# Kernel tuning notes

Measured on AMD Instinct MI355X. Metric: run time of the kernel, lower is better.

Reference implementation:

```python
import jax, jax.numpy as jnp
import numpy as np
import math

H = 16
D = 1024
DH = D // H  # 64


def setup_inputs() -> dict:
    key = jax.random.key(0)
    ks = jax.random.split(key, 11)
    B, N = 2, 2048
    f = lambda k, shape, s=1.0: jax.random.normal(k, shape, dtype=jnp.float32) * s
    return {
        "x_q": f(ks[0], (B, N, D)),
        "x_k": f(ks[1], (B, N, D)),
        "x_v": f(ks[2], (B, N, D)),
        "Wq": f(ks[3], (D, D), 0.02),
        "bq": f(ks[4], (D,), 0.02),
        "Wk": f(ks[5], (D, D), 0.02),
        "bk": f(ks[6], (D,), 0.02),
        "Wv": f(ks[7], (D, D), 0.02),
        "bv": f(ks[8], (D,), 0.02),
        "Wo": f(ks[9], (D, D), 0.02),
        "bo": f(ks[10], (D,), 0.02),
    }


def _mha(x_q, x_k, x_v, Wq, bq, Wk, bk, Wv, bv, Wo, bo):
    B, N, _ = x_q.shape
    # torch nn.Linear: y = x @ W.T + b
    def proj(x, W, b):
        y = x @ W.T + b                      # [B, N, D]
        return y.reshape(B, N, H, DH).transpose(0, 2, 1, 3)  # [B, H, N, DH]
    Q = proj(x_q, Wq, bq)
    K = proj(x_k, Wk, bk)
    V = proj(x_v, Wv, bv)
    scores = jnp.einsum("bhqd,bhkd->bhqk", Q, K) / math.sqrt(DH)  # [B,H,N,N]
    attn = jax.nn.softmax(scores, axis=-1)
    X = jnp.einsum("bhqk,bhkd->bhqd", attn, V)   # [B,H,N,DH]
    X = X.transpose(0, 2, 1, 3).reshape(B, N, D)  # concat heads
    return X @ Wo.T + bo


def reference(x_q, x_k, x_v, Wq, bq, Wk, bk, Wv, bv, Wo, bo):
    return _mha(x_q, x_k, x_v, Wq, bq, Wk, bk, Wv, bv, Wo, bo)
```

## Files before the change

kernel.cpp:

```cpp
#include <hip/hip_runtime.h>

typedef unsigned short u16;
typedef __attribute__((ext_vector_type(8))) short s16x8;
typedef __attribute__((ext_vector_type(4))) float f32x4;
typedef unsigned uint2v __attribute__((ext_vector_type(2)));

#define B_  2
#define N_  2048
#define D_  1024
#define H_  16
#define DH_ 64
#define M_  4096

#define S_X (M_ * D_)
#define S_W (D_ * D_)

#define QSCALE 0.1803368801111204f

#define OFF_QB 0
#define OFF_KB (S_X)
#define OFF_VB (2 * S_X)
#define OFF_XB (3 * S_X)
#define OFF_XQ (4 * S_X)
#define OFF_XK (5 * S_X)
#define OFF_XV (6 * S_X)
#define OFF_WQ (7 * S_X)
#define OFF_WK (7 * S_X + S_W)
#define OFF_WV (7 * S_X + 2 * S_W)
#define OFF_WO (7 * S_X + 3 * S_W)
#define WS_FAST_BYTES ((size_t)(7 * S_X + 4 * S_W) * 2)

#if __has_builtin(__builtin_amdgcn_exp2f)
#define EXP2(x) __builtin_amdgcn_exp2f(x)
#else
#define EXP2(x) exp2f(x)
#endif

__device__ __forceinline__ u16 f2bf(float f) {
  unsigned u = __builtin_bit_cast(unsigned, f);
  u += 0x7fffu + ((u >> 16) & 1u);
  return (u16)(u >> 16);
}
__device__ __forceinline__ s16x8 pack8(float4 a, float4 b) {
  s16x8 r;
  r[0] = (short)f2bf(a.x); r[1] = (short)f2bf(a.y);
  r[2] = (short)f2bf(a.z); r[3] = (short)f2bf(a.w);
  r[4] = (short)f2bf(b.x); r[5] = (short)f2bf(b.y);
  r[6] = (short)f2bf(b.z); r[7] = (short)f2bf(b.w);
  return r;
}
__device__ __forceinline__ void gl2lds16(const void* g, void* l) {
  __builtin_amdgcn_global_load_lds(
      (const __attribute__((address_space(1))) void*)g,
      (__attribute__((address_space(3))) void*)l, 16, 0, 0);
}
__device__ __forceinline__ void pl32(unsigned &a, unsigned &b) {
#if __has_builtin(__builtin_amdgcn_permlane32_swap)
  uint2v r = __builtin_amdgcn_permlane32_swap(a, b, 0, 0);
  a = r[0]; b = r[1];
#else
  asm("v_permlane32_swap_b32 %0, %1" : "+v"(a), "+v"(b));
#endif
}
__device__ __forceinline__ void pl16(unsigned &a, unsigned &b) {
#if __has_builtin(__builtin_amdgcn_permlane16_swap)
  uint2v r = __builtin_amdgcn_permlane16_swap(a, b, 0, 0);
  a = r[0]; b = r[1];
#else
  asm("v_permlane16_swap_b32 %0, %1" : "+v"(a), "+v"(b));
#endif
}

__global__ __launch_bounds__(256)
void cvt_kernel(const float* __restrict__ p0, const float* __restrict__ p1,
                const float* __restrict__ p2, const float* __restrict__ p3,
                const float* __restrict__ p4, const float* __restrict__ p5,
                const float* __restrict__ p6, u16* __restrict__ ws) {
  const float* src; u16* dst; int n;
  switch (blockIdx.y) {
    case 0:  src = p0; dst = ws + OFF_XQ; n = S_X; break;
    case 1:  src = p1; dst = ws + OFF_XK; n = S_X; break;
    case 2:  src = p2; dst = ws + OFF_XV; n = S_X; break;
    case 3:  src = p3; dst = ws + OFF_WQ; n = S_W; break;
    case 4:  src = p4; dst = ws + OFF_WK; n = S_W; break;
    case 5:  src = p5; dst = ws + OFF_WV; n = S_W; break;
    default: src = p6; dst = ws + OFF_WO; n = S_W; break;
  }
  const int stride = gridDim.x * blockDim.x * 4;
  for (int idx = (blockIdx.x * blockDim.x + threadIdx.x) * 4; idx < n; idx += stride) {
    const float4 v = *(const float4*)&src[idx];
    ushort4 o;
    o.x = f2bf(v.x); o.y = f2bf(v.y); o.z = f2bf(v.z); o.w = f2bf(v.w);
    *(ushort4*)&dst[idx] = o;
  }
}

__global__ __launch_bounds__(256, 3)
void qkv_gemm_bf(const u16* __restrict__ ws_in, const float* __restrict__ bq,
                 const float* __restrict__ bk, const float* __restrict__ bv,
                 u16* __restrict__ ws_out) {
  __shared__ __align__(16) u16 As[128 * 32];
  __shared__ __align__(16) u16 Bs[128 * 32];
  __shared__ __align__(16) u16 Ts[128][136];
  const int flat = (blockIdx.z * 32 + blockIdx.y) * 8 + blockIdx.x;
  const int u = flat & 7, v = flat >> 3;
  const int bxn = v & 7;
  const int byz = u * 12 + (v >> 3);
  const int z = byz >> 5, bym = byz & 31;

  const u16* A = ws_in + OFF_XQ + (size_t)z * S_X;
  const u16* W = ws_in + OFF_WQ + (size_t)z * S_W;
  const float* bias = (z == 0) ? bq : (z == 1) ? bk : bv;
  u16* out = ws_out + (size_t)z * S_X;
  const float scale = (z == 0) ? QSCALE : 1.0f;

  const int tid  = threadIdx.x;
  const int wave = tid >> 6, lane = tid & 63;
  const int quad = lane >> 4, l16 = lane & 15;
  const int wr = wave >> 1, wc = wave & 1;
  const int m0 = bym * 128, n0 = bxn * 128;

  f32x4 acc[4][4];
#pragma unroll
  for (int i = 0; i < 4; ++i)
#pragma unroll
    for (int j = 0; j < 4; ++j) acc[i][j] = {0.f, 0.f, 0.f, 0.f};

  for (int kt = 0; kt < D_ / 32; ++kt) {
    const int kb = kt * 32;
#pragma unroll
    for (int call = 0; call < 2; ++call) {
      const int c = call * 256 + wave * 64 + lane;
      const int row = c >> 2, col8 = (c & 3) * 8;
      gl2lds16(&A[(size_t)(m0 + row) * D_ + kb + col8],
               &As[(size_t)(call * 256 + wave * 64) * 8]);
      gl2lds16(&W[(size_t)(n0 + row) * D_ + kb + col8],
               &Bs[(size_t)(call * 256 + wave * 64) * 8]);
    }
    __syncthreads();

    s16x8 af[4], bf[4];
#pragma unroll
    for (int i = 0; i < 4; ++i) {
      af[i] = *(const s16x8*)&As[(wr * 64 + i * 16 + l16) * 32 + quad * 8];
      bf[i] = *(const s16x8*)&Bs[(wc * 64 + i * 16 + l16) * 32 + quad * 8];
    }
#pragma unroll
    for (int i = 0; i < 4; ++i)
#pragma unroll
      for (int j = 0; j < 4; ++j)
        acc[i][j] = __builtin_amdgcn_mfma_f32_16x16x32_bf16(af[i], bf[j], acc[i][j], 0, 0, 0);
    __syncthreads();
  }

  if (z != 2) {
#pragma unroll
    for (int j = 0; j < 4; ++j) {
      const int col = n0 + wc * 64 + j * 16 + l16;
      const float bvv = bias[col];
#pragma unroll
      for (int i = 0; i < 4; ++i) {
        const int row0 = m0 + wr * 64 + i * 16 + quad * 4;
#pragma unroll
        for (int r = 0; r < 4; ++r)
          out[(size_t)(row0 + r) * D_ + col] = f2bf((acc[i][j][r] + bvv) * scale);
      }
    }
  } else {
#pragma unroll
    for (int j = 0; j < 4; ++j) {
      const int cl = wc * 64 + j * 16 + l16;
      const float bvv = bias[n0 + cl];
#pragma unroll
      for (int i = 0; i < 4; ++i) {
        const int tl0 = wr * 64 + i * 16 + quad * 4;
#pragma unroll
        for (int r = 0; r < 4; ++r)
          Ts[cl][tl0 + r] = f2bf(acc[i][j][r] + bvv);
      }
    }
    __syncthreads();
    const int bb = m0 >> 11;
    const int t0 = m0 & (N_ - 1);
#pragma unroll
    for (int it = 0; it < 8; ++it) {
      const int row = it * 16 + (tid >> 4);
      const int seg = tid & 15;
      const int colg = n0 + row;
      const int hh = colg >> 6, dh = colg & 63;
      const s16x8 vv = *(const s16x8*)&Ts[row][seg * 8];
      *(s16x8*)&out[(size_t)((bb * H_ + hh) * DH_ + dh) * N_ + t0 + seg * 8] = vv;
    }
  }
}

__global__ __launch_bounds__(256, 3)
void qkv_gemm_f32(const float* __restrict__ xq, const float* __restrict__ xk,
                  const float* __restrict__ xv, const float* __restrict__ Wq,
                  const float* __restrict__ Wk, const float* __restrict__ Wv,
                  const float* __restrict__ bq, const float* __restrict__ bk,
                  const float* __restrict__ bv, u16* __restrict__ ws) {
  __shared__ __align__(16) u16 As[128 * 32];
  __shared__ __align__(16) u16 Bs[128 * 32];
  const int flat = (blockIdx.z * 32 + blockIdx.y) * 8 + blockIdx.x;
  const int u = flat & 7, v = flat >> 3;
  const int bxn = v & 7;
  const int byz = u * 12 + (v >> 3);
  const int z = byz >> 5, bym = byz & 31;

  const float* A    = (z == 0) ? xq : (z == 1) ? xk : xv;
  const float* W    = (z == 0) ? Wq : (z == 1) ? Wk : Wv;
  const float* bias = (z == 0) ? bq : (z == 1) ? bk : bv;
  u16* out = ws + (size_t)z * S_X;
  const float scale = (z == 0) ? QSCALE : 1.0f;

  const int tid  = threadIdx.x;
  const int wave = tid >> 6, lane = tid & 63;
  const int quad = lane >> 4, l16 = lane & 15;
  const int wr = wave >> 1, wc = wave & 1;
  const int m0 = bym * 128, n0 = bxn * 128;

  f32x4 acc[4][4];
#pragma unroll
  for (int i = 0; i < 4; ++i)
#pragma unroll
    for (int j = 0; j < 4; ++j) acc[i][j] = {0.f, 0.f, 0.f, 0.f};

  for (int kt = 0; kt < D_ / 32; ++kt) {
    const int kb = kt * 32;
#pragma unroll
    for (int call = 0; call < 2; ++call) {
      const int c = call * 256 + wave * 64 + lane;
      const int row = c >> 2, col = (c & 3) * 8;
      const float4 a0 = *(const float4*)&A[(size_t)(m0 + row) * D_ + kb + col];
      const float4 a1 = *(const float4*)&A[(size_t)(m0 + row) * D_ + kb + col + 4];
      const float4 w0 = *(const float4*)&W[(size_t)(n0 + row) * D_ + kb + col];
      const float4 w1 = *(const float4*)&W[(size_t)(n0 + row) * D_ + kb + col + 4];
      *(s16x8*)&As[c * 8] = pack8(a0, a1);
      *(s16x8*)&Bs[c * 8] = pack8(w0, w1);
    }
    __syncthreads();

    s16x8 af[4], bf[4];
#pragma unroll
    for (int i = 0; i < 4; ++i) {
      af[i] = *(const s16x8*)&As[(wr * 64 + i * 16 + l16) * 32 + quad * 8];
      bf[i] = *(const s16x8*)&Bs[(wc * 64 + i * 16 + l16) * 32 + quad * 8];
    }
#pragma unroll
    for (int i = 0; i < 4; ++i)
#pragma unroll
      for (int j = 0; j < 4; ++j)
        acc[i][j] = __builtin_amdgcn_mfma_f32_16x16x32_bf16(af[i], bf[j], acc[i][j], 0, 0, 0);
    __syncthreads();
  }

  if (z != 2) {
#pragma unroll
    for (int j = 0; j < 4; ++j) {
      const int col = n0 + wc * 64 + j * 16 + l16;
      const float bvv = bias[col];
#pragma unroll
      for (int i = 0; i < 4; ++i) {
        const int row0 = m0 + wr * 64 + i * 16 + quad * 4;
#pragma unroll
        for (int r = 0; r < 4; ++r)
          out[(size_t)(row0 + r) * D_ + col] = f2bf((acc[i][j][r] + bvv) * scale);
      }
    }
  } else {
#pragma unroll
    for (int j = 0; j < 4; ++j) {
      const int col = n0 + wc * 64 + j * 16 + l16;
      const int h = col >> 6, dh = col & 63;
      const float bvv = bias[col];
#pragma unroll
      for (int i = 0; i < 4; ++i) {
        const int row0 = m0 + wr * 64 + i * 16 + quad * 4;
#pragma unroll
        for (int r = 0; r < 4; ++r) {
          const int tok = row0 + r;
          const int b = tok >> 11, t = tok & (N_ - 1);
          out[(size_t)((b * H_ + h) * DH_ + dh) * N_ + t] = f2bf(acc[i][j][r] + bvv);
        }
      }
    }
  }
}

__global__ __launch_bounds__(256, 2)
void attn_kernel(const u16* __restrict__ Q, const u16* __restrict__ K,
                 const u16* __restrict__ Vt, u16* __restrict__ X) {
  __shared__ __align__(16) u16 Ks[2][128 * 64];
  __shared__ __align__(16) u16 Vs[2][64 * 128];
  const int tid  = threadIdx.x;
  const int wave = tid >> 6, lane = tid & 63;
  const int quad = lane >> 4, l16 = lane & 15;

  const int flat = blockIdx.y * 16 + blockIdx.x;
  const int u = flat & 7, slot = flat >> 3;
  const int qb = slot & 15;
  const int bh = u * 4 + (slot >> 4);
  const int q0 = qb * 128;
  const int b = bh >> 4, h = bh & 15;

  s16x8 qfa[2], qfb[2];
#pragma unroll
  for (int ks = 0; ks < 2; ++ks) {
    qfa[ks] = *(const s16x8*)&Q[(size_t)(b * N_ + q0 + wave * 16 + l16) * D_ +
                                h * 64 + ks * 32 + quad * 8];
    qfb[ks] = *(const s16x8*)&Q[(size_t)(b * N_ + q0 + 64 + wave * 16 + l16) * D_ +
                                h * 64 + ks * 32 + quad * 8];
  }

  s16x8 onesf;
#pragma unroll
  for (int i = 0; i < 8; ++i) onesf[i] = (short)0x3F80;

  f32x4 oa[4], ob[4];
#pragma unroll
  for (int mt = 0; mt < 4; ++mt) { oa[mt] = {0.f, 0.f, 0.f, 0.f}; ob[mt] = {0.f, 0.f, 0.f, 0.f}; }
  f32x4 la = {0.f, 0.f, 0.f, 0.f}, lb = {0.f, 0.f, 0.f, 0.f};

  auto stage = [&](int buf, int kt) {
    const int k0 = kt * 128;
#pragma unroll
    for (int c4 = 0; c4 < 4; ++c4) {
      const int p = c4 * 256 + wave * 64 + lane;
      { const int row = p >> 3, cd = p & 7, src = cd ^ (row & 7);
        gl2lds16(&K[(size_t)(b * N_ + k0 + row) * D_ + h * 64 + src * 8],
                 &Ks[buf][(size_t)(c4 * 256 + wave * 64) * 8]); }
      { const int row = p >> 4, cd = p & 15;
        const int src = (cd & 8) | ((cd & 7) ^ (row & 7));
        gl2lds16(&Vt[(size_t)((b * H_ + h) * DH_ + row) * N_ + k0 + src * 8],
                 &Vs[buf][(size_t)(c4 * 256 + wave * 64) * 8]); }
    }
  };

  stage(0, 0);
  int cur = 0;

  for (int kt = 0; kt < N_ / 128; ++kt) {
    if (kt + 1 < N_ / 128) {
      stage(cur ^ 1, kt + 1);
      asm volatile("s_waitcnt vmcnt(8)" ::: "memory");
    } else {
      asm volatile("s_waitcnt vmcnt(0)" ::: "memory");
    }
    __builtin_amdgcn_sched_barrier(0);
    __builtin_amdgcn_s_barrier();

    const u16* ks = &Ks[cur][0];
    const u16* vs = &Vs[cur][0];

    f32x4 sa[8], sb[8];
#pragma unroll
    for (int nt = 0; nt < 8; ++nt) { sa[nt] = {0.f, 0.f, 0.f, 0.f}; sb[nt] = {0.f, 0.f, 0.f, 0.f}; }
    __builtin_amdgcn_s_setprio(1);
#pragma unroll
    for (int nt = 0; nt < 8; ++nt) {
      const int row = nt * 16 + l16;
      const s16x8 kf0 = *(const s16x8*)&ks[row * 64 + ((quad    ) ^ (l16 & 7)) * 8];
      const s16x8 kf1 = *(const s16x8*)&ks[row * 64 + ((4 + quad) ^ (l16 & 7)) * 8];
      sa[nt] = __builtin_amdgcn_mfma_f32_16x16x32_bf16(kf0, qfa[0], sa[nt], 0, 0, 0);
      sa[nt] = __builtin_amdgcn_mfma_f32_16x16x32_bf16(kf1, qfa[1], sa[nt], 0, 0, 0);
      sb[nt] = __builtin_amdgcn_mfma_f32_16x16x32_bf16(kf0, qfb[0], sb[nt], 0, 0, 0);
      sb[nt] = __builtin_amdgcn_mfma_f32_16x16x32_bf16(kf1, qfb[1], sb[nt], 0, 0, 0);
    }
    __builtin_amdgcn_s_setprio(0);

    unsigned pka[8][2], pkb[8][2];
#pragma unroll
    for (int nt = 0; nt < 8; ++nt) {
      { const unsigned b0 = __builtin_bit_cast(unsigned, EXP2(sa[nt][0]));
        const unsigned b1 = __builtin_bit_cast(unsigned, EXP2(sa[nt][1]));
        const unsigned b2 = __builtin_bit_cast(unsigned, EXP2(sa[nt][2]));
        const unsigned b3 = __builtin_bit_cast(unsigned, EXP2(sa[nt][3]));
        pka[nt][0] = (b0 >> 16) | (b1 & 0xffff0000u);
        pka[nt][1] = (b2 >> 16) | (b3 & 0xffff0000u); }
      { const unsigned b0 = __builtin_bit_cast(unsigned, EXP2(sb[nt][0]));
        const unsigned b1 = __builtin_bit_cast(unsigned, EXP2(sb[nt][1]));
        const unsigned b2 = __builtin_bit_cast(unsigned, EXP2(sb[nt][2]));
        const unsigned b3 = __builtin_bit_cast(unsigned, EXP2(sb[nt][3]));
        pkb[nt][0] = (b0 >> 16) | (b1 & 0xffff0000u);
        pkb[nt][1] = (b2 >> 16) | (b3 & 0xffff0000u); }
    }

#pragma unroll
    for (int k2 = 0; k2 < 4; ++k2) {
      s16x8 vf[4];
#pragma unroll
      for (int mt = 0; mt < 4; ++mt) {
        const int row = mt * 16 + l16;
        const int j8 = k2 * 4 + quad;
        const int cd = (j8 & 8) | ((j8 & 7) ^ (row & 7));
        vf[mt] = *(const s16x8*)&vs[row * 128 + cd * 8];
      }
      unsigned Aa0 = pka[k2 * 2][0], Ba0 = pka[k2 * 2 + 1][0];
      unsigned Aa1 = pka[k2 * 2][1], Ba1 = pka[k2 * 2 + 1][1];
      pl32(Aa0, Ba0); pl16(Aa0, Ba0);
      pl32(Aa1, Ba1); pl16(Aa1, Ba1);
      int4 bda; bda.x = (int)Aa0; bda.y = (int)Aa1; bda.z = (int)Ba0; bda.w = (int)Ba1;
      unsigned Ab0 = pkb[k2 * 2][0], Bb0 = pkb[k2 * 2 + 1][0];
      unsigned Ab1 = pkb[k2 * 2][1], Bb1 = pkb[k2 * 2 + 1][1];
      pl32(Ab0, Bb0); pl16(Ab0, Bb0);
      pl32(Ab1, Bb1); pl16(Ab1, Bb1);
      int4 bdb; bdb.x = (int)Ab0; bdb.y = (int)Ab1; bdb.z = (int)Bb0; bdb.w = (int)Bb1;
      const s16x8 bfa = __builtin_bit_cast(s16x8, bda);
      const s16x8 bfb = __builtin_bit_cast(s16x8, bdb);
      __builtin_amdgcn_s_setprio(1);
#pragma unroll
      for (int mt = 0; mt < 4; ++mt) {
        oa[mt] = __builtin_amdgcn_mfma_f32_16x16x32_bf16(vf[mt], bfa, oa[mt], 0, 0, 0);
        ob[mt] = __builtin_amdgcn_mfma_f32_16x16x32_bf16(vf[mt], bfb, ob[mt], 0, 0, 0);
      }
      la = __builtin_amdgcn_mfma_f32_16x16x32_bf16(onesf, bfa, la, 0, 0, 0);
      lb = __builtin_amdgcn_mfma_f32_16x16x32_bf16(onesf, bfb, lb, 0, 0, 0);
      __builtin_amdgcn_s_setprio(0);
    }

    asm volatile("s_waitcnt lgkmcnt(0)" ::: "memory");
    __builtin_amdgcn_s_barrier();
    cur ^= 1;
  }

  const float inva = 1.0f / la[0];
  const float invb = 1.0f / lb[0];
  const int qa = q0 + wave * 16 + l16;
#pragma unroll
  for (int mt = 0; mt < 4; ++mt) {
    ushort4 w;
    w.x = f2bf(oa[mt][0] * inva);
    w.y = f2bf(oa[mt][1] * inva);
    w.z = f2bf(oa[mt][2] * inva);
    w.w = f2bf(oa[mt][3] * inva);
    *(ushort4*)&X[(size_t)(b * N_ + qa) * D_ + h * 64 + mt * 16 + quad * 4] = w;
  }
#pragma unroll
  for (int mt = 0; mt < 4; ++mt) {
    ushort4 w;
    w.x = f2bf(ob[mt][0] * invb);
    w.y = f2bf(ob[mt][1] * invb);
    w.z = f2bf(ob[mt][2] * invb);
    w.w = f2bf(ob[mt][3] * invb);
    *(ushort4*)&X[(size_t)(b * N_ + qa + 64) * D_ + h * 64 + mt * 16 + quad * 4] = w;
  }
}

__global__ __launch_bounds__(256, 2)
void out_gemm_bf(const u16* __restrict__ A, const u16* __restrict__ W,
                 const float* __restrict__ bias, float* __restrict__ out) {
  __shared__ __align__(16) u16 As[64 * 32];
  __shared__ __align__(16) u16 Bs[128 * 32];
  const int tid  = threadIdx.x;
  const int wave = tid >> 6, lane = tid & 63;
  const int quad = lane >> 4, l16 = lane & 15;
  const int wr = wave >> 1, wc = wave & 1;

  const int flat = blockIdx.y * 8 + blockIdx.x;
  const int u = flat & 7, v = flat >> 3;
  const int bxn = v & 7;
  const int bym = u * 8 + (v >> 3);
  const int m0 = bym * 64, n0 = bxn * 128;

  f32x4 acc[2][4];
#pragma unroll
  for (int i = 0; i < 2; ++i)
#pragma unroll
    for (int j = 0; j < 4; ++j) acc[i][j] = {0.f, 0.f, 0.f, 0.f};

  for (int kt = 0; kt < D_ / 32; ++kt) {
    const int kb = kt * 32;
    { const int c = wave * 64 + lane;
      const int row = c >> 2, col8 = (c & 3) * 8;
      gl2lds16(&A[(size_t)(m0 + row) * D_ + kb + col8], &As[(size_t)(wave * 64) * 8]); }
#pragma unroll
    for (int call = 0; call < 2; ++call) {
      const int c = call * 256 + wave * 64 + lane;
      const int row = c >> 2, col8 = (c & 3) * 8;
      gl2lds16(&W[(size_t)(n0 + row) * D_ + kb + col8],
               &Bs[(size_t)(call * 256 + wave * 64) * 8]);
    }
    __syncthreads();

    s16x8 af[2], bf[4];
#pragma unroll
    for (int i = 0; i < 2; ++i)
      af[i] = *(const s16x8*)&As[(wr * 32 + i * 16 + l16) * 32 + quad * 8];
#pragma unroll
    for (int j = 0; j < 4; ++j)
      bf[j] = *(const s16x8*)&Bs[(wc * 64 + j * 16 + l16) * 32 + quad * 8];
#pragma unroll
    for (int i = 0; i < 2; ++i)
#pragma unroll
      for (int j = 0; j < 4; ++j)
        acc[i][j] = __builtin_amdgcn_mfma_f32_16x16x32_bf16(af[i], bf[j], acc[i][j], 0, 0, 0);
    __syncthreads();
  }

#pragma unroll
  for (int j = 0; j < 4; ++j) {
    const int col = n0 + wc * 64 + j * 16 + l16;
    const float bv = bias[col];
#pragma unroll
    for (int i = 0; i < 2; ++i) {
      const int row0 = m0 + wr * 32 + i * 16 + quad * 4;
#pragma unroll
      for (int r = 0; r < 4; ++r)
        out[(size_t)(row0 + r) * D_ + col] = acc[i][j][r] + bv;
    }
  }
}

__global__ __launch_bounds__(256, 2)
void out_gemm_f32(const u16* __restrict__ A, const float* __restrict__ W,
                  const float* __restrict__ bias, float* __restrict__ out) {
  __shared__ __align__(16) u16 As[64 * 32];
  __shared__ __align__(16) u16 Bs[128 * 32];
  const int tid  = threadIdx.x;
  const int wave = tid >> 6, lane = tid & 63;
  const int quad = lane >> 4, l16 = lane & 15;
  const int wr = wave >> 1, wc = wave & 1;

  const int flat = blockIdx.y * 8 + blockIdx.x;
  const int u = flat & 7, v = flat >> 3;
  const int bxn = v & 7;
  const int bym = u * 8 + (v >> 3);
  const int m0 = bym * 64, n0 = bxn * 128;

  f32x4 acc[2][4];
#pragma unroll
  for (int i = 0; i < 2; ++i)
#pragma unroll
    for (int j = 0; j < 4; ++j) acc[i][j] = {0.f, 0.f, 0.f, 0.f};

  for (int kt = 0; kt < D_ / 32; ++kt) {
    const int kb = kt * 32;
    { const int c = wave * 64 + lane;
      const int row = c >> 2, col = (c & 3) * 8;
      gl2lds16(&A[(size_t)(m0 + row) * D_ + kb + col], &As[(size_t)(wave * 64) * 8]); }
#pragma unroll
    for (int call = 0; call < 2; ++call) {
      const int c = call * 256 + wave * 64 + lane;
      const int row = c >> 2, col = (c & 3) * 8;
      const float4 w0 = *(const float4*)&W[(size_t)(n0 + row) * D_ + kb + col];
      const float4 w1 = *(const float4*)&W[(size_t)(n0 + row) * D_ + kb + col + 4];
      *(s16x8*)&Bs[c * 8] = pack8(w0, w1);
    }
    __syncthreads();

    s16x8 af[2], bf[4];
#pragma unroll
    for (int i = 0; i < 2; ++i)
      af[i] = *(const s16x8*)&As[(wr * 32 + i * 16 + l16) * 32 + quad * 8];
#pragma unroll
    for (int j = 0; j < 4; ++j)
      bf[j] = *(const s16x8*)&Bs[(wc * 64 + j * 16 + l16) * 32 + quad * 8];
#pragma unroll
    for (int i = 0; i < 2; ++i)
#pragma unroll
      for (int j = 0; j < 4; ++j)
        acc[i][j] = __builtin_amdgcn_mfma_f32_16x16x32_bf16(af[i], bf[j], acc[i][j], 0, 0, 0);
    __syncthreads();
  }

#pragma unroll
  for (int j = 0; j < 4; ++j) {
    const int col = n0 + wc * 64 + j * 16 + l16;
    const float bv = bias[col];
#pragma unroll
    for (int i = 0; i < 2; ++i) {
      const int row0 = m0 + wr * 32 + i * 16 + quad * 4;
#pragma unroll
      for (int r = 0; r < 4; ++r)
        out[(size_t)(row0 + r) * D_ + col] = acc[i][j][r] + bv;
    }
  }
}

extern "C" void kernel_launch(void* const* d_in, const int* in_sizes, int n_in,
                              void* d_out, int out_size, void* d_ws, size_t ws_size,
                              hipStream_t stream) {
  const float* xq = (const float*)d_in[0];
  const float* xk = (const float*)d_in[1];
  const float* xv = (const float*)d_in[2];
  const float* Wq = (const float*)d_in[3];
  const float* bq = (const float*)d_in[4];
  const float* Wk = (const float*)d_in[5];
  const float* bk = (const float*)d_in[6];
  const float* Wv = (const float*)d_in[7];
  const float* bv = (const float*)d_in[8];
  const float* Wo = (const float*)d_in[9];
  const float* bo = (const float*)d_in[10];
  u16*   ws  = (u16*)d_ws;
  float* out = (float*)d_out;

  dim3 blk(256);
  if (ws_size >= WS_FAST_BYTES) {
    hipLaunchKernelGGL(cvt_kernel, dim3(256, 7), blk, 0, stream,
                       xq, xk, xv, Wq, Wk, Wv, Wo, ws);
    hipLaunchKernelGGL(qkv_gemm_bf, dim3(8, 32, 3), blk, 0, stream,
                       ws, bq, bk, bv, ws + OFF_QB);
    hipLaunchKernelGGL(attn_kernel, dim3(16, 32), blk, 0, stream,
                       ws + OFF_QB, ws + OFF_KB, ws + OFF_VB, ws + OFF_XB);
    hipLaunchKernelGGL(out_gemm_bf, dim3(8, 64), blk, 0, stream,
                       ws + OFF_XB, ws + OFF_WO, bo, out);
  } else {
    hipLaunchKernelGGL(qkv_gemm_f32, dim3(8, 32, 3), blk, 0, stream,
                       xq, xk, xv, Wq, Wk, Wv, bq, bk, bv, ws);
    hipLaunchKernelGGL(attn_kernel, dim3(16, 32), blk, 0, stream,
                       ws + OFF_QB, ws + OFF_KB, ws + OFF_VB, ws + OFF_XB);
    hipLaunchKernelGGL(out_gemm_f32, dim3(8, 64), blk, 0, stream,
                       ws + OFF_XB, Wo, bo, out);
  }
}
```

Baseline: 209.8 us.

## Drop bf16 pre-conversion path and stage V transpose through LDS in f32 GEMM

Removes the separate f32-to-bf16 conversion kernel and the bf16-input GEMMs, so the QKV and output projections always read f32 inputs directly. The f32 QKV GEMM now writes V through an LDS transpose tile, producing coalesced 16-byte stores instead of scattered 2-byte stores. This saves one kernel launch and a full pass over the inputs. In exchange, the GEMMs convert to bf16 inside their inner loops and the QKV kernel uses more shared memory, which can lower occupancy.

```diff
diff --git a/kernel.cpp b/kernel.cpp
--- a/kernel.cpp
+++ b/kernel.cpp
@@ -21,14 +21,6 @@
 #define OFF_KB (S_X)
 #define OFF_VB (2 * S_X)
 #define OFF_XB (3 * S_X)
-#define OFF_XQ (4 * S_X)
-#define OFF_XK (5 * S_X)
-#define OFF_XV (6 * S_X)
-#define OFF_WQ (7 * S_X)
-#define OFF_WK (7 * S_X + S_W)
-#define OFF_WV (7 * S_X + 2 * S_W)
-#define OFF_WO (7 * S_X + 3 * S_W)
-#define WS_FAST_BYTES ((size_t)(7 * S_X + 4 * S_W) * 2)
 
 #if __has_builtin(__builtin_amdgcn_exp2f)
 #define EXP2(x) __builtin_amdgcn_exp2f(x)
@@ -69,129 +61,6 @@
 #else
   asm("v_permlane16_swap_b32 %0, %1" : "+v"(a), "+v"(b));
 #endif
-}
-
-__global__ __launch_bounds__(256)
-void cvt_kernel(const float* __restrict__ p0, const float* __restrict__ p1,
-                const float* __restrict__ p2, const float* __restrict__ p3,
-                const float* __restrict__ p4, const float* __restrict__ p5,
-                const float* __restrict__ p6, u16* __restrict__ ws) {
-  const float* src; u16* dst; int n;
-  switch (blockIdx.y) {
-    case 0:  src = p0; dst = ws + OFF_XQ; n = S_X; break;
-    case 1:  src = p1; dst = ws + OFF_XK; n = S_X; break;
-    case 2:  src = p2; dst = ws + OFF_XV; n = S_X; break;
-    case 3:  src = p3; dst = ws + OFF_WQ; n = S_W; break;
-    case 4:  src = p4; dst = ws + OFF_WK; n = S_W; break;
-    case 5:  src = p5; dst = ws + OFF_WV; n = S_W; break;
-    default: src = p6; dst = ws + OFF_WO; n = S_W; break;
-  }
-  const int stride = gridDim.x * blockDim.x * 4;
-  for (int idx = (blockIdx.x * blockDim.x + threadIdx.x) * 4; idx < n; idx += stride) {
-    const float4 v = *(const float4*)&src[idx];
-    ushort4 o;
-    o.x = f2bf(v.x); o.y = f2bf(v.y); o.z = f2bf(v.z); o.w = f2bf(v.w);
-    *(ushort4*)&dst[idx] = o;
-  }
-}
-
-__global__ __launch_bounds__(256, 3)
-void qkv_gemm_bf(const u16* __restrict__ ws_in, const float* __restrict__ bq,
-                 const float* __restrict__ bk, const float* __restrict__ bv,
-                 u16* __restrict__ ws_out) {
-  __shared__ __align__(16) u16 As[128 * 32];
-  __shared__ __align__(16) u16 Bs[128 * 32];
-  __shared__ __align__(16) u16 Ts[128][136];
-  const int flat = (blockIdx.z * 32 + blockIdx.y) * 8 + blockIdx.x;
-  const int u = flat & 7, v = flat >> 3;
-  const int bxn = v & 7;
-  const int byz = u * 12 + (v >> 3);
-  const int z = byz >> 5, bym = byz & 31;
-
-  const u16* A = ws_in + OFF_XQ + (size_t)z * S_X;
-  const u16* W = ws_in + OFF_WQ + (size_t)z * S_W;
-  const float* bias = (z == 0) ? bq : (z == 1) ? bk : bv;
-  u16* out = ws_out + (size_t)z * S_X;
-  const float scale = (z == 0) ? QSCALE : 1.0f;
-
-  const int tid  = threadIdx.x;
-  const int wave = tid >> 6, lane = tid & 63;
-  const int quad = lane >> 4, l16 = lane & 15;
-  const int wr = wave >> 1, wc = wave & 1;
-  const int m0 = bym * 128, n0 = bxn * 128;
-
-  f32x4 acc[4][4];
-#pragma unroll
-  for (int i = 0; i < 4; ++i)
-#pragma unroll
-    for (int j = 0; j < 4; ++j) acc[i][j] = {0.f, 0.f, 0.f, 0.f};
-
-  for (int kt = 0; kt < D_ / 32; ++kt) {
-    const int kb = kt * 32;
-#pragma unroll
-    for (int call = 0; call < 2; ++call) {
-      const int c = call * 256 + wave * 64 + lane;
-      const int row = c >> 2, col8 = (c & 3) * 8;
-      gl2lds16(&A[(size_t)(m0 + row) * D_ + kb + col8],
-               &As[(size_t)(call * 256 + wave * 64) * 8]);
-      gl2lds16(&W[(size_t)(n0 + row) * D_ + kb + col8],
-               &Bs[(size_t)(call * 256 + wave * 64) * 8]);
-    }
-    __syncthreads();
-
-    s16x8 af[4], bf[4];
-#pragma unroll
-    for (int i = 0; i < 4; ++i) {
-      af[i] = *(const s16x8*)&As[(wr * 64 + i * 16 + l16) * 32 + quad * 8];
-      bf[i] = *(const s16x8*)&Bs[(wc * 64 + i * 16 + l16) * 32 + quad * 8];
-    }
-#pragma unroll
-    for (int i = 0; i < 4; ++i)
-#pragma unroll
-      for (int j = 0; j < 4; ++j)
-        acc[i][j] = __builtin_amdgcn_mfma_f32_16x16x32_bf16(af[i], bf[j], acc[i][j], 0, 0, 0);
-    __syncthreads();
-  }
-
-  if (z != 2) {
-#pragma unroll
-    for (int j = 0; j < 4; ++j) {
-      const int col = n0 + wc * 64 + j * 16 + l16;
-      const float bvv = bias[col];
-#pragma unroll
-      for (int i = 0; i < 4; ++i) {
-        const int row0 = m0 + wr * 64 + i * 16 + quad * 4;
-#pragma unroll
-        for (int r = 0; r < 4; ++r)
-          out[(size_t)(row0 + r) * D_ + col] = f2bf((acc[i][j][r] + bvv) * scale);
-      }
-    }
-  } else {
-#pragma unroll
-    for (int j = 0; j < 4; ++j) {
-      const int cl = wc * 64 + j * 16 + l16;
-      const float bvv = bias[n0 + cl];
-#pragma unroll
-      for (int i = 0; i < 4; ++i) {
-        const int tl0 = wr * 64 + i * 16 + quad * 4;
-#pragma unroll
-        for (int r = 0; r < 4; ++r)
-          Ts[cl][tl0 + r] = f2bf(acc[i][j][r] + bvv);
-      }
-    }
-    __syncthreads();
-    const int bb = m0 >> 11;
-    const int t0 = m0 & (N_ - 1);
-#pragma unroll
-    for (int it = 0; it < 8; ++it) {
-      const int row = it * 16 + (tid >> 4);
-      const int seg = tid & 15;
-      const int colg = n0 + row;
-      const int hh = colg >> 6, dh = colg & 63;
-      const s16x8 vv = *(const s16x8*)&Ts[row][seg * 8];
-      *(s16x8*)&out[(size_t)((bb * H_ + hh) * DH_ + dh) * N_ + t0 + seg * 8] = vv;
-    }
-  }
 }
 
 __global__ __launch_bounds__(256, 3)
@@ -202,6 +71,7 @@
                   const float* __restrict__ bv, u16* __restrict__ ws) {
   __shared__ __align__(16) u16 As[128 * 32];
   __shared__ __align__(16) u16 Bs[128 * 32];
+  __shared__ __align__(16) u16 Ts[128][136];
   const int flat = (blockIdx.z * 32 + blockIdx.y) * 8 + blockIdx.x;
   const int u = flat & 7, v = flat >> 3;
   const int bxn = v & 7;
@@ -271,19 +141,27 @@
   } else {
 #pragma unroll
     for (int j = 0; j < 4; ++j) {
-      const int col = n0 + wc * 64 + j * 16 + l16;
-      const int h = col >> 6, dh = col & 63;
-      const float bvv = bias[col];
+      const int cl = wc * 64 + j * 16 + l16;
+      const float bvv = bias[n0 + cl];
 #pragma unroll
       for (int i = 0; i < 4; ++i) {
-        const int row0 = m0 + wr * 64 + i * 16 + quad * 4;
-#pragma unroll
-        for (int r = 0; r < 4; ++r) {
-          const int tok = row0 + r;
-          const int b = tok >> 11, t = tok & (N_ - 1);
-          out[(size_t)((b * H_ + h) * DH_ + dh) * N_ + t] = f2bf(acc[i][j][r] + bvv);
-        }
+        const int tl0 = wr * 64 + i * 16 + quad * 4;
+#pragma unroll
+        for (int r = 0; r < 4; ++r)
+          Ts[cl][tl0 + r] = f2bf(acc[i][j][r] + bvv);
       }
+    }
+    __syncthreads();
+    const int bb = m0 >> 11;
+    const int t0 = m0 & (N_ - 1);
+#pragma unroll
+    for (int it = 0; it < 8; ++it) {
+      const int row = it * 16 + (tid >> 4);
+      const int seg = tid & 15;
+      const int colg = n0 + row;
+      const int hh = colg >> 6, dh = colg & 63;
+      const s16x8 vv = *(const s16x8*)&Ts[row][seg * 8];
+      *(s16x8*)&out[(size_t)((bb * H_ + hh) * DH_ + dh) * N_ + t0 + seg * 8] = vv;
     }
   }
 }
@@ -448,71 +326,6 @@
 }
 
 __global__ __launch_bounds__(256, 2)
-void out_gemm_bf(const u16* __restrict__ A, const u16* __restrict__ W,
-                 const float* __restrict__ bias, float* __restrict__ out) {
-  __shared__ __align__(16) u16 As[64 * 32];
-  __shared__ __align__(16) u16 Bs[128 * 32];
-  const int tid  = threadIdx.x;
-  const int wave = tid >> 6, lane = tid & 63;
-  const int quad = lane >> 4, l16 = lane & 15;
-  const int wr = wave >> 1, wc = wave & 1;
-
-  const int flat = blockIdx.y * 8 + blockIdx.x;
-  const int u = flat & 7, v = flat >> 3;
-  const int bxn = v & 7;
-  const int bym = u * 8 + (v >> 3);
-  const int m0 = bym * 64, n0 = bxn * 128;
-
-  f32x4 acc[2][4];
-#pragma unroll
-  for (int i = 0; i < 2; ++i)
-#pragma unroll
-    for (int j = 0; j < 4; ++j) acc[i][j] = {0.f, 0.f, 0.f, 0.f};
-
-  for (int kt = 0; kt < D_ / 32; ++kt) {
-    const int kb = kt * 32;
-    { const int c = wave * 64 + lane;
-      const int row = c >> 2, col8 = (c & 3) * 8;
-      gl2lds16(&A[(size_t)(m0 + row) * D_ + kb + col8], &As[(size_t)(wave * 64) * 8]); }
-#pragma unroll
-    for (int call = 0; call < 2; ++call) {
-      const int c = call * 256 + wave * 64 + lane;
-      const int row = c >> 2, col8 = (c & 3) * 8;
-      gl2lds16(&W[(size_t)(n0 + row) * D_ + kb + col8],
-               &Bs[(size_t)(call * 256 + wave * 64) * 8]);
-    }
-    __syncthreads();
-
-    s16x8 af[2], bf[4];
-#pragma unroll
-    for (int i = 0; i < 2; ++i)
-      af[i] = *(const s16x8*)&As[(wr * 32 + i * 16 + l16) * 32 + quad * 8];
-#pragma unroll
-    for (int j = 0; j < 4; ++j)
-      bf[j] = *(const s16x8*)&Bs[(wc * 64 + j * 16 + l16) * 32 + quad * 8];
-#pragma unroll
-    for (int i = 0; i < 2; ++i)
-#pragma unroll
-      for (int j = 0; j < 4; ++j)
-        acc[i][j] = __builtin_amdgcn_mfma_f32_16x16x32_bf16(af[i], bf[j], acc[i][j], 0, 0, 0);
-    __syncthreads();
-  }
-
-#pragma unroll
-  for (int j = 0; j < 4; ++j) {
-    const int col = n0 + wc * 64 + j * 16 + l16;
-    const float bv = bias[col];
-#pragma unroll
-    for (int i = 0; i < 2; ++i) {
-      const int row0 = m0 + wr * 32 + i * 16 + quad * 4;
-#pragma unroll
-      for (int r = 0; r < 4; ++r)
-        out[(size_t)(row0 + r) * D_ + col] = acc[i][j][r] + bv;
-    }
-  }
-}
-
-__global__ __launch_bounds__(256, 2)
 void out_gemm_f32(const u16* __restrict__ A, const float* __restrict__ W,
                   const float* __restrict__ bias, float* __restrict__ out) {
   __shared__ __align__(16) u16 As[64 * 32];
@@ -596,21 +409,10 @@
   float* out = (float*)d_out;
 
   dim3 blk(256);
-  if (ws_size >= WS_FAST_BYTES) {
-    hipLaunchKernelGGL(cvt_kernel, dim3(256, 7), blk, 0, stream,
-                       xq, xk, xv, Wq, Wk, Wv, Wo, ws);
-    hipLaunchKernelGGL(qkv_gemm_bf, dim3(8, 32, 3), blk, 0, stream,
-                       ws, bq, bk, bv, ws + OFF_QB);
-    hipLaunchKernelGGL(attn_kernel, dim3(16, 32), blk, 0, stream,
-                       ws + OFF_QB, ws + OFF_KB, ws + OFF_VB, ws + OFF_XB);
-    hipLaunchKernelGGL(out_gemm_bf, dim3(8, 64), blk, 0, stream,
-                       ws + OFF_XB, ws + OFF_WO, bo, out);
-  } else {
-    hipLaunchKernelGGL(qkv_gemm_f32, dim3(8, 32, 3), blk, 0, stream,
-                       xq, xk, xv, Wq, Wk, Wv, bq, bk, bv, ws);
-    hipLaunchKernelGGL(attn_kernel, dim3(16, 32), blk, 0, stream,
-                       ws + OFF_QB, ws + OFF_KB, ws + OFF_VB, ws + OFF_XB);
-    hipLaunchKernelGGL(out_gemm_f32, dim3(8, 64), blk, 0, stream,
-                       ws + OFF_XB, Wo, bo, out);
-  }
-}
+  hipLaunchKernelGGL(qkv_gemm_f32, dim3(8, 32, 3), blk, 0, stream,
+                     xq, xk, xv, Wq, Wk, Wv, bq, bk, bv, ws);
+  hipLaunchKernelGGL(attn_kernel, dim3(16, 32), blk, 0, stream,
+                     ws + OFF_QB, ws + OFF_KB, ws + OFF_VB, ws + OFF_XB);
+  hipLaunchKernelGGL(out_gemm_f32, dim3(8, 64), blk, 0, stream,
+                     ws + OFF_XB, Wo, bo, out);
+}
```

After: 266.1 us. 1.27x slower.
